# Kernel tuning notes

Measured on AMD Instinct MI355X. Metric: run time of the kernel, lower is better.

The kernel has to match this reference:

```python
import jax, jax.numpy as jnp
import numpy as np

B, S, D, H, DK, FF = 2, 2048, 1024, 16, 64, 4096
EPS = 1e-6


def _layernorm(x, g, b):
    m = jnp.mean(x, axis=-1, keepdims=True)
    v = jnp.mean((x - m) ** 2, axis=-1, keepdims=True)
    return (x - m) * jax.lax.rsqrt(v + EPS) * g + b


def setup_inputs() -> dict:
    key = jax.random.key(0)
    ks = jax.random.split(key, 20)
    sc = 0.02
    rn = lambda k, sh: (jax.random.normal(k, sh, jnp.float32) * sc)
    return {
        "inputs": jax.random.normal(ks[0], (B, S, D), jnp.float32),
        "wq": rn(ks[1], (D, H * DK)), "bq": jnp.zeros((H * DK,), jnp.float32),
        "wk": rn(ks[2], (D, H * DK)), "bk": jnp.zeros((H * DK,), jnp.float32),
        "wv": rn(ks[3], (D, H * DK)), "bv": jnp.zeros((H * DK,), jnp.float32),
        "wo": rn(ks[4], (H * DK, D)), "bo": jnp.zeros((D,), jnp.float32),
        "ln1_g": jnp.ones((D,), jnp.float32), "ln1_b": jnp.zeros((D,), jnp.float32),
        "wi0": rn(ks[5], (D, FF)), "bi0": jnp.zeros((FF,), jnp.float32),
        "wi1": rn(ks[6], (D, FF)), "bi1": jnp.zeros((FF,), jnp.float32),
        "wff": rn(ks[7], (FF, D)), "bff": jnp.zeros((D,), jnp.float32),
        "ln2_g": jnp.ones((D,), jnp.float32), "ln2_b": jnp.zeros((D,), jnp.float32),
    }


def reference(inputs, wq, bq, wk, bk, wv, bv, wo, bo, ln1_g, ln1_b,
              wi0, bi0, wi1, bi1, wff, bff, ln2_g, ln2_b):
    # --- pre-norm MHA block ---
    h = _layernorm(inputs, ln1_g, ln1_b)
    q = (h @ wq + bq).reshape(B, S, H, DK)
    k = (h @ wk + bk).reshape(B, S, H, DK)
    v = (h @ wv + bv).reshape(B, S, H, DK)
    scores = jnp.einsum('bqhd,bkhd->bhqk', q, k) / jnp.sqrt(jnp.float32(DK))
    attn = jax.nn.softmax(scores, axis=-1)                 # [B,H,S,S]
    ctx = jnp.einsum('bhqk,bkhd->bqhd', attn, v).reshape(B, S, H * DK)
    h1 = inputs + (ctx @ wo + bo)
    # --- pre-norm GeGLU FFN block ---
    h2 = _layernorm(h1, ln2_g, ln2_b)
    hg = jax.nn.gelu(h2 @ wi0 + bi0, approximate=False)
    hl = h2 @ wi1 + bi1
    out = h1 + ((hg * hl) @ wff + bff)
    return out, attn
```

## Files before the change

kernel.cpp:

```cpp
#include <hip/hip_runtime.h>
#include <hip/hip_bf16.h>
#include <cstdint>

#define DEV __device__ __forceinline__

typedef __bf16 bf16_t;
typedef __bf16 bf16x8 __attribute__((ext_vector_type(8)));
typedef __bf16 bf16x4 __attribute__((ext_vector_type(4)));
typedef float  f32x4  __attribute__((ext_vector_type(4)));

constexpr int Bb = 2, Ss = 2048, Dd = 1024, Hh = 16, DKk = 64, FFf = 4096;
constexpr int TOK = Bb * Ss;
constexpr float LN_EPS = 1e-6f;

DEV void g2l16(const void* g, void* l) {
    __builtin_amdgcn_global_load_lds(
        (const __attribute__((address_space(1))) unsigned int*)g,
        (__attribute__((address_space(3))) unsigned int*)l, 16, 0, 0);
}

#define WAITCNT(N) asm volatile("s_waitcnt vmcnt(" #N ")" ::: "memory")
#define SCHEDB() __builtin_amdgcn_sched_barrier(0)

__global__ __launch_bounds__(256)
void transpose_cast(const float* __restrict__ src, bf16_t* __restrict__ dst,
                    int K, int N) {
    __shared__ float t[32][33];
    const int tx = threadIdx.x & 31, ty = threadIdx.x >> 5;
    const int n0 = blockIdx.x * 32, k0 = blockIdx.y * 32;
#pragma unroll
    for (int i = 0; i < 4; ++i)
        t[ty + 8 * i][tx] = src[(size_t)(k0 + ty + 8 * i) * N + n0 + tx];
    __syncthreads();
#pragma unroll
    for (int i = 0; i < 4; ++i)
        dst[(size_t)(n0 + ty + 8 * i) * K + k0 + tx] = (bf16_t)t[tx][ty + 8 * i];
}

__global__ __launch_bounds__(256)
void concat3(const float* __restrict__ a, const float* __restrict__ b,
             const float* __restrict__ c, float* __restrict__ o) {
    const int i = blockIdx.x * 256 + threadIdx.x;
    o[i] = a[i]; o[1024 + i] = b[i]; o[2048 + i] = c[i];
}
__global__ __launch_bounds__(256)
void concat2(const float* __restrict__ a, const float* __restrict__ b,
             float* __restrict__ o) {
    const int i = blockIdx.x * 256 + threadIdx.x;
    o[i] = a[i]; o[4096 + i] = b[i];
}

__global__ __launch_bounds__(256)
void ln_fwd(const float* __restrict__ x, const float* __restrict__ g,
            const float* __restrict__ b, bf16_t* __restrict__ out) {
    __shared__ float red[8];
    const int row = blockIdx.x, tid = threadIdx.x;
    const float4 v = ((const float4*)(x + (size_t)row * Dd))[tid];
    float s  = v.x + v.y + v.z + v.w;
    float sq = v.x * v.x + v.y * v.y + v.z * v.z + v.w * v.w;
#pragma unroll
    for (int o = 32; o; o >>= 1) { s += __shfl_xor(s, o); sq += __shfl_xor(sq, o); }
    if ((tid & 63) == 0) { red[tid >> 6] = s; red[4 + (tid >> 6)] = sq; }
    __syncthreads();
    s  = red[0] + red[1] + red[2] + red[3];
    sq = red[4] + red[5] + red[6] + red[7];
    const float mean = s * (1.f / Dd);
    const float var  = sq * (1.f / Dd) - mean * mean;
    const float rs   = rsqrtf(var + LN_EPS);
    const float4 gv = ((const float4*)g)[tid];
    const float4 bv = ((const float4*)b)[tid];
    bf16x4 o4;
    o4[0] = (bf16_t)((v.x - mean) * rs * gv.x + bv.x);
    o4[1] = (bf16_t)((v.y - mean) * rs * gv.y + bv.y);
    o4[2] = (bf16_t)((v.z - mean) * rs * gv.z + bv.z);
    o4[3] = (bf16_t)((v.w - mean) * rs * gv.w + bv.w);
    ((bf16x4*)(out + (size_t)row * Dd))[tid] = o4;
}

template <int EPI>
DEV void gemm_epi(float val, int gr, int gc, int N,
                  void* outp, void* out2, void* out3, const float* resid) {
    if constexpr (EPI == 0) {
        ((bf16_t*)outp)[(size_t)gr * N + gc] = (bf16_t)val;
    } else if constexpr (EPI == 1) {
        const size_t idx = (size_t)gr * N + gc;
        ((float*)outp)[idx] = val + resid[idx];
    } else {
        const int sel = gc >> 10, col = gc & 1023;
        if (sel == 0) {
            ((bf16_t*)outp)[(size_t)gr * 1024 + col] = (bf16_t)val;
        } else if (sel == 1) {
            ((bf16_t*)out2)[(size_t)gr * 1024 + col] = (bf16_t)val;
        } else {
            const int bb = gr >> 11, sS = gr & 2047;
            ((bf16_t*)out3)[((size_t)bb << 21) + ((size_t)col << 11) + sS] = (bf16_t)val;
        }
    }
}

template <int BM, int BN, int EPI>
__global__ __launch_bounds__(256)
void gemm_t(const bf16_t* __restrict__ A, const bf16_t* __restrict__ Bt,
            const float* __restrict__ bias, const float* __restrict__ resid,
            void* __restrict__ outp, void* __restrict__ out2,
            void* __restrict__ out3, int M, int N, int K) {
    constexpr int WM = BM / 2, WN = BN / 2;
    constexpr int MI = WM / 16, NI = WN / 16;
    constexpr int CA = BM / 32, CB = BN / 32;
    __shared__ bf16_t As[BM * 64];
    __shared__ bf16_t Bs[BN * 64];
    const int tid = threadIdx.x;
    const int lane = tid & 63;
    const int wave = tid >> 6;
    const int wr = wave >> 1, wc = wave & 1;
    const int m0 = blockIdx.y * BM, n0 = blockIdx.x * BN;
    const int lr = lane & 15, lg = lane >> 4;

    const f32x4 z0 = {0.f, 0.f, 0.f, 0.f};
    f32x4 acc[MI][NI];
#pragma unroll
    for (int i = 0; i < MI; ++i)
#pragma unroll
        for (int j = 0; j < NI; ++j) acc[i][j] = z0;

    for (int k0 = 0; k0 < K; k0 += 64) {
#pragma unroll
        for (int c = 0; c < CA; ++c) {
            const int lin = c * 256 + tid;
            const int row = lin >> 3, col = (lin & 7) * 8;
            g2l16(A + (size_t)(m0 + row) * K + k0 + col, (char*)As + lin * 16);
        }
#pragma unroll
        for (int c = 0; c < CB; ++c) {
            const int lin = c * 256 + tid;
            const int row = lin >> 3, col = (lin & 7) * 8;
            g2l16(Bt + (size_t)(n0 + row) * K + k0 + col, (char*)Bs + lin * 16);
        }
        __syncthreads();

        bf16x8 af[2][MI], bw[2][NI];
#pragma unroll
        for (int kk = 0; kk < 2; ++kk)
#pragma unroll
            for (int mi = 0; mi < MI; ++mi)
                af[kk][mi] = *(const bf16x8*)(As + (wr * WM + mi * 16 + lr) * 64 +
                                              kk * 32 + lg * 8);
#pragma unroll
        for (int kk = 0; kk < 2; ++kk)
#pragma unroll
            for (int ni = 0; ni < NI; ++ni)
                bw[kk][ni] = *(const bf16x8*)(Bs + (wc * WN + ni * 16 + lr) * 64 +
                                              kk * 32 + lg * 8);
#pragma unroll
        for (int mi = 0; mi < MI; ++mi)
#pragma unroll
            for (int ni = 0; ni < NI; ++ni) {
                acc[mi][ni] = __builtin_amdgcn_mfma_f32_16x16x32_bf16(
                    af[0][mi], bw[0][ni], acc[mi][ni], 0, 0, 0);
                acc[mi][ni] = __builtin_amdgcn_mfma_f32_16x16x32_bf16(
                    af[1][mi], bw[1][ni], acc[mi][ni], 0, 0, 0);
            }
        __syncthreads();
    }

#pragma unroll
    for (int mi = 0; mi < MI; ++mi)
#pragma unroll
        for (int ni = 0; ni < NI; ++ni) {
            const int gc = n0 + wc * WN + ni * 16 + lr;
            const int gr0 = m0 + wr * WM + mi * 16 + lg * 4;
            const float bvl = bias[gc];
#pragma unroll
            for (int r = 0; r < 4; ++r)
                gemm_epi<EPI>(acc[mi][ni][r] + bvl, gr0 + r, gc, N, outp, out2, out3, resid);
        }
}

__global__ __launch_bounds__(256)
void attn_fused(const bf16_t* __restrict__ q, const bf16_t* __restrict__ k,
                const bf16_t* __restrict__ vT, float* __restrict__ attn,
                bf16_t* __restrict__ ctx) {
    __shared__ bf16_t Ks[3][64 * 64];
    __shared__ bf16_t Vs[3][64 * 64];
    const int tid = threadIdx.x, lane = tid & 63, wave = tid >> 6;
    const int lr = lane & 15, lg = lane >> 4;
    int blk = blockIdx.x;
    blk = (blk & 7) * 128 + (blk >> 3);
    const int qc = blk & 31, bh = blk >> 5;
    const int b = bh >> 4, h = bh & 15;
    const int q0 = qc * 64 + wave * 16;
    const size_t base = (size_t)b * (Ss * 1024) + h * 64;
    constexpr float SCL = 0.125f * 1.4426950408889634f;
    const f32x4 z0 = {0.f, 0.f, 0.f, 0.f};

    const int st_r8 = lane >> 3;
    const int st_c0 = (lane & 7) ^ (st_r8 & 3);

    const bf16x8 aq0 = *(const bf16x8*)(q + base + (size_t)(q0 + lr) * 1024 + lg * 8);
    const bf16x8 aq1 = *(const bf16x8*)(q + base + (size_t)(q0 + lr) * 1024 + 32 + lg * 8);
    const bf16_t* kb = k + base;
    const bf16_t* vb_base = vT + ((size_t)bh * 64) * Ss;

#define STAGE_K(kt_, buf_)                                                        \
    {                                                                             \
        _Pragma("unroll")                                                         \
        for (int i = 0; i < 2; ++i)                                               \
            g2l16(kb + (size_t)((kt_) * 64 + wave * 16 + i * 8 + st_r8) * 1024 +  \
                      (st_c0 ^ (i * 4)) * 8,                                      \
                  &Ks[buf_][wave * 1024 + i * 512]);                              \
    }
#define STAGE_V(kt_, buf_)                                                        \
    {                                                                             \
        _Pragma("unroll")                                                         \
        for (int i = 0; i < 2; ++i)                                               \
            g2l16(vb_base + (size_t)(wave * 16 + i * 8 + st_r8) * Ss +            \
                      (kt_) * 64 + (st_c0 ^ (i * 4)) * 8,                         \
                  &Vs[buf_][wave * 1024 + i * 512]);                              \
    }

    f32x4 ea = z0, eb = z0;
    STAGE_K(0, 0);
    STAGE_K(1, 1);
    for (int kt = 0; kt < 32; ++kt) {
        const int buf = kt % 3;
        if (kt == 31) { WAITCNT(0); } else { WAITCNT(2); }
        SCHEDB();
        __builtin_amdgcn_s_barrier();
        SCHEDB();
        f32x4 sa[4];
        __builtin_amdgcn_s_setprio(1);
#pragma unroll
        for (int ct = 0; ct < 4; ++ct) {
            const int ar = ct * 16 + lr;
            const int hz = (ar & 3) | (((ar >> 3) & 1) << 2);
            bf16x8 k0 = *(const bf16x8*)&Ks[buf][ar * 64 + (lg ^ hz) * 8];
            bf16x8 k1 = *(const bf16x8*)&Ks[buf][ar * 64 + (((4 + lg) ^ hz)) * 8];
            sa[ct] = __builtin_amdgcn_mfma_f32_16x16x32_bf16(k0, aq0, z0, 0, 0, 0);
            sa[ct] = __builtin_amdgcn_mfma_f32_16x16x32_bf16(k1, aq1, sa[ct], 0, 0, 0);
        }
        __builtin_amdgcn_s_setprio(0);
#pragma unroll
        for (int r = 0; r < 4; ++r) {
            ea[r] += exp2f(sa[0][r] * SCL) + exp2f(sa[1][r] * SCL);
            eb[r] += exp2f(sa[2][r] * SCL) + exp2f(sa[3][r] * SCL);
        }
        if (kt + 2 < 32) STAGE_K(kt + 2, (kt + 2) % 3);
    }
    float e = ((ea[0] + ea[1]) + (ea[2] + ea[3])) + ((eb[0] + eb[1]) + (eb[2] + eb[3]));
    e += __shfl_xor(e, 16);
    e += __shfl_xor(e, 32);
    const float invl = 1.f / e;

    f32x4 cacc[4];
#pragma unroll
    for (int nd = 0; nd < 4; ++nd) cacc[nd] = z0;

    float* attn_base = attn + ((size_t)bh * Ss + q0 + lr) * Ss;

    __builtin_amdgcn_s_barrier();
    SCHEDB();

    STAGE_K(0, 0); STAGE_V(0, 0);
    STAGE_K(1, 1); STAGE_V(1, 1);
    for (int kt = 0; kt < 32; ++kt) {
        const int buf = kt % 3;
        if (kt == 0 || kt == 31) { WAITCNT(4); } else { WAITCNT(8); }
        SCHEDB();
        __builtin_amdgcn_s_barrier();
        SCHEDB();
#pragma unroll
        for (int kp = 0; kp < 2; ++kp) {
            bf16x8 pa;
            __builtin_amdgcn_s_setprio(1);
#pragma unroll
            for (int ch = 0; ch < 2; ++ch) {
                const int pr = kp * 32 + (lr >> 2) * 8 + ch * 4 + (lr & 3);
                const int hz = (pr & 3) | (((pr >> 3) & 1) << 2);
                bf16x8 k0 = *(const bf16x8*)&Ks[buf][pr * 64 + (lg ^ hz) * 8];
                bf16x8 k1 = *(const bf16x8*)&Ks[buf][pr * 64 + (((4 + lg) ^ hz)) * 8];
                f32x4 sb = __builtin_amdgcn_mfma_f32_16x16x32_bf16(k0, aq0, z0, 0, 0, 0);
                sb = __builtin_amdgcn_mfma_f32_16x16x32_bf16(k1, aq1, sb, 0, 0, 0);
                float4 p;
                p.x = exp2f(sb[0] * SCL) * invl;
                p.y = exp2f(sb[1] * SCL) * invl;
                p.z = exp2f(sb[2] * SCL) * invl;
                p.w = exp2f(sb[3] * SCL) * invl;
                *(float4*)(attn_base + kt * 64 + kp * 32 + lg * 8 + ch * 4) = p;
                pa[ch * 4 + 0] = (bf16_t)p.x;
                pa[ch * 4 + 1] = (bf16_t)p.y;
                pa[ch * 4 + 2] = (bf16_t)p.z;
                pa[ch * 4 + 3] = (bf16_t)p.w;
            }
#pragma unroll
            for (int nd = 0; nd < 4; ++nd) {
                const int vr = nd * 16 + lr;
                const int hv = (vr & 3) | (((vr >> 3) & 1) << 2);
                bf16x8 vb = *(const bf16x8*)&Vs[buf][vr * 64 + (((kp * 4 + lg) ^ hv)) * 8];
                cacc[nd] = __builtin_amdgcn_mfma_f32_16x16x32_bf16(pa, vb, cacc[nd], 0, 0, 0);
            }
            __builtin_amdgcn_s_setprio(0);
        }
        if (kt + 2 < 32) {
            const int nb = (kt + 2) % 3;
            STAGE_K(kt + 2, nb);
            STAGE_V(kt + 2, nb);
        }
    }
#pragma unroll
    for (int nd = 0; nd < 4; ++nd)
#pragma unroll
        for (int r = 0; r < 4; ++r)
            ctx[((size_t)b * Ss + q0 + lg * 4 + r) * 1024 + h * 64 + nd * 16 + lr] =
                (bf16_t)cacc[nd][r];
#undef STAGE_K
#undef STAGE_V
}

__global__ __launch_bounds__(256)
void geglu_kernel(const bf16_t* __restrict__ hgl, bf16_t* __restrict__ g) {
    const int row = blockIdx.y;
    const int c = (blockIdx.x * 256 + threadIdx.x) * 8;
    const size_t rb = (size_t)row * 8192;
    bf16x8 a  = *(const bf16x8*)(hgl + rb + c);
    bf16x8 cc = *(const bf16x8*)(hgl + rb + 4096 + c);
    bf16x8 o;
#pragma unroll
    for (int j = 0; j < 8; ++j) {
        const float x = (float)a[j];
        const float y = (float)cc[j];
        o[j] = (bf16_t)(0.5f * x * (1.f + erff(x * 0.70710678118654752f)) * y);
    }
    *(bf16x8*)(g + (size_t)row * 4096 + c) = o;
}

extern "C" void kernel_launch(void* const* d_in, const int* in_sizes, int n_in,
                              void* d_out, int out_size, void* d_ws, size_t ws_size,
                              hipStream_t stream) {
    const float* inp  = (const float*)d_in[0];
    const float* wq   = (const float*)d_in[1];
    const float* bq   = (const float*)d_in[2];
    const float* wk   = (const float*)d_in[3];
    const float* bk   = (const float*)d_in[4];
    const float* wv   = (const float*)d_in[5];
    const float* bv   = (const float*)d_in[6];
    const float* wo   = (const float*)d_in[7];
    const float* bo   = (const float*)d_in[8];
    const float* ln1g = (const float*)d_in[9];
    const float* ln1b = (const float*)d_in[10];
    const float* wi0  = (const float*)d_in[11];
    const float* bi0  = (const float*)d_in[12];
    const float* wi1  = (const float*)d_in[13];
    const float* bi1  = (const float*)d_in[14];
    const float* wff  = (const float*)d_in[15];
    const float* bff  = (const float*)d_in[16];
    const float* ln2g = (const float*)d_in[17];
    const float* ln2b = (const float*)d_in[18];

    const size_t M1 = 1u << 20;
    bf16_t* wsb  = (bf16_t*)d_ws;
    bf16_t* wqT  = wsb + 0 * M1;
    bf16_t* wkT  = wsb + 1 * M1;
    bf16_t* wvT  = wsb + 2 * M1;
    bf16_t* woT  = wsb + 3 * M1;
    bf16_t* wi0T = wsb + 4 * M1;
    bf16_t* wi1T = wsb + 8 * M1;
    bf16_t* wffT = wsb + 12 * M1;
    bf16_t* hbuf = wsb + 16 * M1;
    bf16_t* qbuf = wsb + 20 * M1;
    bf16_t* kbuf = wsb + 24 * M1;
    bf16_t* vTb  = wsb + 28 * M1;
    bf16_t* ctxb = wsb + 32 * M1;
    float*  h1   = (float*)(wsb + 36 * M1);
    bf16_t* hgl  = wsb + 44 * M1;
    bf16_t* gbuf = wsb + 20 * M1;
    float*  cb   = (float*)(wsb + 32 * M1);
    float*  cb2  = (float*)(wsb + 32 * M1);

    float* out  = (float*)d_out;
    float* attn = out + (size_t)TOK * Dd;

    transpose_cast<<<dim3(1024 / 32, 1024 / 32), 256, 0, stream>>>(wq, wqT, 1024, 1024);
    transpose_cast<<<dim3(1024 / 32, 1024 / 32), 256, 0, stream>>>(wk, wkT, 1024, 1024);
    transpose_cast<<<dim3(1024 / 32, 1024 / 32), 256, 0, stream>>>(wv, wvT, 1024, 1024);
    transpose_cast<<<dim3(1024 / 32, 1024 / 32), 256, 0, stream>>>(wo, woT, 1024, 1024);
    transpose_cast<<<dim3(4096 / 32, 1024 / 32), 256, 0, stream>>>(wi0, wi0T, 1024, 4096);
    transpose_cast<<<dim3(4096 / 32, 1024 / 32), 256, 0, stream>>>(wi1, wi1T, 1024, 4096);
    transpose_cast<<<dim3(1024 / 32, 4096 / 32), 256, 0, stream>>>(wff, wffT, 4096, 1024);

    concat3<<<4, 256, 0, stream>>>(bq, bk, bv, cb);

    ln_fwd<<<TOK, 256, 0, stream>>>(inp, ln1g, ln1b, hbuf);

    gemm_t<64, 64, 3><<<dim3(48, 64), 256, 0, stream>>>(hbuf, wqT, cb, nullptr,
                                                        qbuf, kbuf, vTb, TOK, 3072, 1024);

    attn_fused<<<Bb * Hh * (Ss / 64), 256, 0, stream>>>(qbuf, kbuf, vTb, attn, ctxb);

    gemm_t<64, 64, 1><<<dim3(16, 64), 256, 0, stream>>>(ctxb, woT, bo, inp, h1,
                                                        nullptr, nullptr, TOK, 1024, 1024);

    concat2<<<16, 256, 0, stream>>>(bi0, bi1, cb2);

    ln_fwd<<<TOK, 256, 0, stream>>>(h1, ln2g, ln2b, hbuf);

    gemm_t<128, 128, 0><<<dim3(64, 32), 256, 0, stream>>>(hbuf, wi0T, cb2, nullptr, hgl,
                                                          nullptr, nullptr, TOK, 8192, 1024);

    geglu_kernel<<<dim3(2, 4096), 256, 0, stream>>>(hgl, gbuf);

    gemm_t<64, 64, 1><<<dim3(16, 64), 256, 0, stream>>>(gbuf, wffT, bff, h1, out,
                                                        nullptr, nullptr, TOK, 1024, 4096);
}
```

Baseline: 539.1 us.

## Fuse GeGLU into dual-B GEMM, batch weight transposes, enlarge QKV tiles

Replaces the wide wi0/wi1 GEMM plus separate GeGLU kernel with one GEMM that accumulates both projections per tile and applies erf-GELU times linear in the epilogue. This avoids writing and rereading the 8192-wide intermediate. It also merges the seven weight transpose launches into one grid and switches the QKV GEMM to 128x128 tiles. The new fused GEMM is a simple single-buffered loop with no load/compute overlap and no LDS swizzle, so it may be slower per FLOP than the tuned gemm_t.

```diff
diff --git a/kernel.cpp b/kernel.cpp
--- a/kernel.cpp
+++ b/kernel.cpp
@@ -23,11 +23,29 @@
 #define SCHEDB() __builtin_amdgcn_sched_barrier(0)
 
 __global__ __launch_bounds__(256)
-void transpose_cast(const float* __restrict__ src, bf16_t* __restrict__ dst,
-                    int K, int N) {
+void transpose_all(const float* __restrict__ wq, const float* __restrict__ wk,
+                   const float* __restrict__ wv, const float* __restrict__ wo,
+                   const float* __restrict__ wi0, const float* __restrict__ wi1,
+                   const float* __restrict__ wff,
+                   bf16_t* wqT, bf16_t* wkT, bf16_t* wvT, bf16_t* woT,
+                   bf16_t* wi0T, bf16_t* wi1T, bf16_t* wffT) {
     __shared__ float t[32][33];
+    const int id = blockIdx.x;
+    const float* src; bf16_t* dst; int K, N, tt;
+    if (id < 4096) {
+        const int w = id >> 10; tt = id & 1023; K = 1024; N = 1024;
+        src = w == 0 ? wq : w == 1 ? wk : w == 2 ? wv : wo;
+        dst = w == 0 ? wqT : w == 1 ? wkT : w == 2 ? wvT : woT;
+    } else if (id < 12288) {
+        const int w = (id - 4096) >> 12; tt = (id - 4096) & 4095; K = 1024; N = 4096;
+        src = w ? wi1 : wi0; dst = w ? wi1T : wi0T;
+    } else {
+        tt = id - 12288; K = 4096; N = 1024;
+        src = wff; dst = wffT;
+    }
+    const int ntn = N >> 5;
+    const int n0 = (tt % ntn) * 32, k0 = (tt / ntn) * 32;
     const int tx = threadIdx.x & 31, ty = threadIdx.x >> 5;
-    const int n0 = blockIdx.x * 32, k0 = blockIdx.y * 32;
 #pragma unroll
     for (int i = 0; i < 4; ++i)
         t[ty + 8 * i][tx] = src[(size_t)(k0 + ty + 8 * i) * N + n0 + tx];
@@ -42,12 +60,6 @@
              const float* __restrict__ c, float* __restrict__ o) {
     const int i = blockIdx.x * 256 + threadIdx.x;
     o[i] = a[i]; o[1024 + i] = b[i]; o[2048 + i] = c[i];
-}
-__global__ __launch_bounds__(256)
-void concat2(const float* __restrict__ a, const float* __restrict__ b,
-             float* __restrict__ o) {
-    const int i = blockIdx.x * 256 + threadIdx.x;
-    o[i] = a[i]; o[4096 + i] = b[i];
 }
 
 __global__ __launch_bounds__(256)
@@ -177,6 +189,95 @@
 }
 
 __global__ __launch_bounds__(256)
+void gemm_geglu(const bf16_t* __restrict__ A, const bf16_t* __restrict__ Bg,
+                const bf16_t* __restrict__ Bl, const float* __restrict__ bi0,
+                const float* __restrict__ bi1, bf16_t* __restrict__ gout) {
+    __shared__ bf16_t As[128 * 64];
+    __shared__ bf16_t Bgs[64 * 64];
+    __shared__ bf16_t Bls[64 * 64];
+    const int tid = threadIdx.x;
+    const int lane = tid & 63;
+    const int wave = tid >> 6;
+    const int wr = wave >> 1, wc = wave & 1;
+    const int m0 = blockIdx.y * 128, n0 = blockIdx.x * 64;
+    const int lr = lane & 15, lg = lane >> 4;
+
+    const f32x4 z0 = {0.f, 0.f, 0.f, 0.f};
+    f32x4 ag[4][2], al[4][2];
+#pragma unroll
+    for (int i = 0; i < 4; ++i)
+#pragma unroll
+        for (int j = 0; j < 2; ++j) { ag[i][j] = z0; al[i][j] = z0; }
+
+    for (int k0 = 0; k0 < 1024; k0 += 64) {
+#pragma unroll
+        for (int c = 0; c < 4; ++c) {
+            const int lin = c * 256 + tid;
+            const int row = lin >> 3, col = (lin & 7) * 8;
+            g2l16(A + (size_t)(m0 + row) * 1024 + k0 + col, (char*)As + lin * 16);
+        }
+#pragma unroll
+        for (int c = 0; c < 2; ++c) {
+            const int lin = c * 256 + tid;
+            const int row = lin >> 3, col = (lin & 7) * 8;
+            g2l16(Bg + (size_t)(n0 + row) * 1024 + k0 + col, (char*)Bgs + lin * 16);
+        }
+#pragma unroll
+        for (int c = 0; c < 2; ++c) {
+            const int lin = c * 256 + tid;
+            const int row = lin >> 3, col = (lin & 7) * 8;
+            g2l16(Bl + (size_t)(n0 + row) * 1024 + k0 + col, (char*)Bls + lin * 16);
+        }
+        __syncthreads();
+
+        bf16x8 af[2][4], bg[2][2], bl[2][2];
+#pragma unroll
+        for (int kk = 0; kk < 2; ++kk) {
+#pragma unroll
+            for (int mi = 0; mi < 4; ++mi)
+                af[kk][mi] = *(const bf16x8*)(As + (wr * 64 + mi * 16 + lr) * 64 +
+                                              kk * 32 + lg * 8);
+#pragma unroll
+            for (int ni = 0; ni < 2; ++ni) {
+                bg[kk][ni] = *(const bf16x8*)(Bgs + (wc * 32 + ni * 16 + lr) * 64 +
+                                              kk * 32 + lg * 8);
+                bl[kk][ni] = *(const bf16x8*)(Bls + (wc * 32 + ni * 16 + lr) * 64 +
+                                              kk * 32 + lg * 8);
+            }
+        }
+#pragma unroll
+        for (int mi = 0; mi < 4; ++mi)
+#pragma unroll
+            for (int ni = 0; ni < 2; ++ni) {
+#pragma unroll
+                for (int kk = 0; kk < 2; ++kk) {
+                    ag[mi][ni] = __builtin_amdgcn_mfma_f32_16x16x32_bf16(
+                        af[kk][mi], bg[kk][ni], ag[mi][ni], 0, 0, 0);
+                    al[mi][ni] = __builtin_amdgcn_mfma_f32_16x16x32_bf16(
+                        af[kk][mi], bl[kk][ni], al[mi][ni], 0, 0, 0);
+                }
+            }
+        __syncthreads();
+    }
+
+#pragma unroll
+    for (int mi = 0; mi < 4; ++mi)
+#pragma unroll
+        for (int ni = 0; ni < 2; ++ni) {
+            const int gc = n0 + wc * 32 + ni * 16 + lr;
+            const int gr0 = m0 + wr * 64 + mi * 16 + lg * 4;
+            const float b0 = bi0[gc], b1 = bi1[gc];
+#pragma unroll
+            for (int r = 0; r < 4; ++r) {
+                const float x = ag[mi][ni][r] + b0;
+                const float y = al[mi][ni][r] + b1;
+                const float ge = 0.5f * x * (1.f + erff(x * 0.70710678118654752f));
+                gout[(size_t)(gr0 + r) * 4096 + gc] = (bf16_t)(ge * y);
+            }
+        }
+}
+
+__global__ __launch_bounds__(256)
 void attn_fused(const bf16_t* __restrict__ q, const bf16_t* __restrict__ k,
                 const bf16_t* __restrict__ vT, float* __restrict__ attn,
                 bf16_t* __restrict__ ctx) {
@@ -314,23 +415,6 @@
                 (bf16_t)cacc[nd][r];
 #undef STAGE_K
 #undef STAGE_V
-}
-
-__global__ __launch_bounds__(256)
-void geglu_kernel(const bf16_t* __restrict__ hgl, bf16_t* __restrict__ g) {
-    const int row = blockIdx.y;
-    const int c = (blockIdx.x * 256 + threadIdx.x) * 8;
-    const size_t rb = (size_t)row * 8192;
-    bf16x8 a  = *(const bf16x8*)(hgl + rb + c);
-    bf16x8 cc = *(const bf16x8*)(hgl + rb + 4096 + c);
-    bf16x8 o;
-#pragma unroll
-    for (int j = 0; j < 8; ++j) {
-        const float x = (float)a[j];
-        const float y = (float)cc[j];
-        o[j] = (bf16_t)(0.5f * x * (1.f + erff(x * 0.70710678118654752f)) * y);
-    }
-    *(bf16x8*)(g + (size_t)row * 4096 + c) = o;
 }
 
 extern "C" void kernel_launch(void* const* d_in, const int* in_sizes, int n_in,
@@ -371,42 +455,30 @@
     bf16_t* vTb  = wsb + 28 * M1;
     bf16_t* ctxb = wsb + 32 * M1;
     float*  h1   = (float*)(wsb + 36 * M1);
-    bf16_t* hgl  = wsb + 44 * M1;
-    bf16_t* gbuf = wsb + 20 * M1;
-    float*  cb   = (float*)(wsb + 32 * M1);
-    float*  cb2  = (float*)(wsb + 32 * M1);
+    bf16_t* gbuf = wsb + 44 * M1;
+    float*  cb   = (float*)(wsb + 60 * M1);
 
     float* out  = (float*)d_out;
     float* attn = out + (size_t)TOK * Dd;
 
-    transpose_cast<<<dim3(1024 / 32, 1024 / 32), 256, 0, stream>>>(wq, wqT, 1024, 1024);
-    transpose_cast<<<dim3(1024 / 32, 1024 / 32), 256, 0, stream>>>(wk, wkT, 1024, 1024);
-    transpose_cast<<<dim3(1024 / 32, 1024 / 32), 256, 0, stream>>>(wv, wvT, 1024, 1024);
-    transpose_cast<<<dim3(1024 / 32, 1024 / 32), 256, 0, stream>>>(wo, woT, 1024, 1024);
-    transpose_cast<<<dim3(4096 / 32, 1024 / 32), 256, 0, stream>>>(wi0, wi0T, 1024, 4096);
-    transpose_cast<<<dim3(4096 / 32, 1024 / 32), 256, 0, stream>>>(wi1, wi1T, 1024, 4096);
-    transpose_cast<<<dim3(1024 / 32, 4096 / 32), 256, 0, stream>>>(wff, wffT, 4096, 1024);
+    transpose_all<<<16384, 256, 0, stream>>>(wq, wk, wv, wo, wi0, wi1, wff,
+                                             wqT, wkT, wvT, woT, wi0T, wi1T, wffT);
 
     concat3<<<4, 256, 0, stream>>>(bq, bk, bv, cb);
 
     ln_fwd<<<TOK, 256, 0, stream>>>(inp, ln1g, ln1b, hbuf);
 
-    gemm_t<64, 64, 3><<<dim3(48, 64), 256, 0, stream>>>(hbuf, wqT, cb, nullptr,
-                                                        qbuf, kbuf, vTb, TOK, 3072, 1024);
+    gemm_t<128, 128, 3><<<dim3(24, 32), 256, 0, stream>>>(hbuf, wqT, cb, nullptr,
+                                                          qbuf, kbuf, vTb, TOK, 3072, 1024);
 
     attn_fused<<<Bb * Hh * (Ss / 64), 256, 0, stream>>>(qbuf, kbuf, vTb, attn, ctxb);
 
     gemm_t<64, 64, 1><<<dim3(16, 64), 256, 0, stream>>>(ctxb, woT, bo, inp, h1,
                                                         nullptr, nullptr, TOK, 1024, 1024);
 
-    concat2<<<16, 256, 0, stream>>>(bi0, bi1, cb2);
-
     ln_fwd<<<TOK, 256, 0, stream>>>(h1, ln2g, ln2b, hbuf);
 
-    gemm_t<128, 128, 0><<<dim3(64, 32), 256, 0, stream>>>(hbuf, wi0T, cb2, nullptr, hgl,
-                                                          nullptr, nullptr, TOK, 8192, 1024);
-
-    geglu_kernel<<<dim3(2, 4096), 256, 0, stream>>>(hgl, gbuf);
+    gemm_geglu<<<dim3(64, 32), 256, 0, stream>>>(hbuf, wi0T, wi1T, bi0, bi1, gbuf);
 
     gemm_t<64, 64, 1><<<dim3(16, 64), 256, 0, stream>>>(gbuf, wffT, bff, h1, out,
                                                         nullptr, nullptr, TOK, 1024, 4096);
```

New measurement: 510.3 us. 1.06x faster.
